# Kernel tuning notes

Measured on AMD Instinct MI355X. Metric: run time of the kernel, lower is better.

The kernel has to match this reference:

```python
import jax, jax.numpy as jnp
import numpy as np
from jax import lax

MU = 0.1          # cfg MODEL.MU (FISTA step size)
LMBD = 0.1        # cfg MODEL.LAMBDA[0]
N_STEPS = 4       # cfg MODEL.NUM_LAYERS (unrolled FISTA iterations)
BN_EPS = 1e-5


def _norm_w(W):
    # DictBlock w_norm: each dictionary filter normalized to unit L2 norm.
    # torch does this under no_grad (in-place on .data), so the norm is a constant.
    n = jnp.sqrt(jnp.sum(W * W, axis=(1, 2, 3), keepdims=True))
    return W / lax.stop_gradient(n + 1e-12)


def _conv(x, W, stride, pad):
    return lax.conv_general_dilated(x, W, (stride, stride), [(pad, pad)] * 2,
                                    dimension_numbers=('NCHW', 'OIHW', 'NCHW'))


def _conv_t(z, W, stride, pad, out_pad):
    # torch conv_transpose2d(z, W, stride, padding=pad, output_padding=out_pad)
    k = W.shape[2]
    Wt = jnp.transpose(jnp.flip(W, (2, 3)), (1, 0, 2, 3))  # (in_ch, dict, k, k)
    p = k - 1 - pad
    return lax.conv_general_dilated(z, Wt, (1, 1), [(p, p + out_pad)] * 2,
                                    lhs_dilation=(stride, stride),
                                    dimension_numbers=('NCHW', 'OIHW', 'NCHW'))


def _shrink(c):
    # non-negative soft threshold: relu(c - lmbd*step)
    return jax.nn.relu(c - LMBD * MU)


def _dict_conv(x, W, stride):
    # Unrolled FISTA sparse coding: min_c 0.5||x - W^T c||^2 + lmbd||c||_1, c>=0
    W = _norm_w(W)
    out_pad = stride - 1
    c = _shrink(MU * _conv(x, W, stride, 1))
    c_pre = jnp.zeros_like(c)
    t = 1.0
    for _ in range(N_STEPS - 1):
        t_next = (1.0 + float(np.sqrt(1.0 + 4.0 * t * t))) / 2.0
        a = c + ((t - 1.0) / t_next) * (c - c_pre)
        c_pre = c
        r = x - _conv_t(a, W, stride, 1, out_pad)       # reconstruction residual
        c = _shrink(a + MU * _conv(r, W, stride, 1))    # proximal gradient step
        t = t_next
    return c


def _bn(x, g, b, m, v):
    # eval-mode BatchNorm2d with running stats
    scale = g * lax.rsqrt(v + BN_EPS)
    return (x - m[None, :, None, None]) * scale[None, :, None, None] + b[None, :, None, None]


def setup_inputs() -> dict:
    key = jax.random.key(0)
    ks = jax.random.split(key, 12)
    N, Cin, Cout, H = 32, 128, 256, 56
    x = jax.random.normal(ks[0], (N, Cin, H, H), jnp.float32)
    def unit_norm(W):
        return W / (jnp.sqrt(jnp.sum(W * W, axis=(1, 2, 3), keepdims=True)) + 1e-12)
    W1 = unit_norm(jax.random.normal(ks[1], (Cout, Cin, 3, 3), jnp.float32))
    W2 = unit_norm(jax.random.normal(ks[2], (Cout, Cout, 3, 3), jnp.float32))
    Wsc = jax.random.normal(ks[3], (Cout, Cin, 1, 1), jnp.float32) * 0.05
    def bn(k):
        k1, k2, k3, k4 = jax.random.split(k, 4)
        g = 1.0 + 0.1 * jax.random.normal(k1, (Cout,), jnp.float32)
        b = 0.1 * jax.random.normal(k2, (Cout,), jnp.float32)
        m = 0.1 * jax.random.normal(k3, (Cout,), jnp.float32)
        v = 0.5 + jax.random.uniform(k4, (Cout,), jnp.float32)
        return g, b, m, v
    bn1_g, bn1_b, bn1_m, bn1_v = bn(ks[4])
    bn2_g, bn2_b, bn2_m, bn2_v = bn(ks[5])
    bnsc_g, bnsc_b, bnsc_m, bnsc_v = bn(ks[6])
    return dict(x=x, W1=W1, W2=W2, Wsc=Wsc,
                bn1_g=bn1_g, bn1_b=bn1_b, bn1_m=bn1_m, bn1_v=bn1_v,
                bn2_g=bn2_g, bn2_b=bn2_b, bn2_m=bn2_m, bn2_v=bn2_v,
                bnsc_g=bnsc_g, bnsc_b=bnsc_b, bnsc_m=bnsc_m, bnsc_v=bnsc_v)


def reference(x, W1, W2, Wsc,
              bn1_g, bn1_b, bn1_m, bn1_v,
              bn2_g, bn2_b, bn2_m, bn2_v,
              bnsc_g, bnsc_b, bnsc_m, bnsc_v):
    out = _bn(_dict_conv(x, W1, 2), bn1_g, bn1_b, bn1_m, bn1_v)
    out = _bn(_dict_conv(out, W2, 1), bn2_g, bn2_b, bn2_m, bn2_v)
    sc = _bn(_conv(x, Wsc, 2, 0), bnsc_g, bnsc_b, bnsc_m, bnsc_v)
    return jax.nn.relu(out + sc)
```

## Files before the change

### kernel.cpp

```cpp
#include <hip/hip_runtime.h>
#include <math.h>

#define MU_F 0.1f
#define SHRINK_F 0.01f
#define BN_EPS_F 1e-5f

typedef _Float16 half_t;
typedef _Float16 half8 __attribute__((ext_vector_type(8)));
typedef float f32x4 __attribute__((ext_vector_type(4)));

#define LROW 40

template<int KS, int S, int PAD, int MODE>
__global__ __launch_bounds__(256, 2)
void conv_big(const half_t* __restrict__ Ag, const half_t* __restrict__ Xh,
              float* __restrict__ outF, half_t* __restrict__ outH,
              const half_t* __restrict__ auxH, const float* __restrict__ auxF,
              int CA, int Cout, int Hin, int Win, int Hout, int Wout, int ptiles,
              float alpha, float beta, float delta, int relu1,
              const float* __restrict__ pscale, const float* __restrict__ pbias,
              const float* __restrict__ aux3, int relu2)
{
    __shared__ __align__(16) half_t sm[2 * 256 * LROW];

    const int tid = threadIdx.x;
    const int wv = tid >> 6, ln = tid & 63;
    const int n = blockIdx.z;
    const int co0 = blockIdx.y * 128;
    const int wco = (wv & 1) * 64, wpx = (wv >> 1) * 64;

    int eh = 0, ew = 0, p0;
    if (MODE == 2) {
        int q = blockIdx.x / ptiles;
        p0 = (blockIdx.x - q * ptiles) * 128;
        eh = q >> 1; ew = q & 1;
    } else {
        p0 = blockIdx.x * 128;
    }

    const int Wd  = (MODE == 2) ? (Wout >> 1) : Wout;
    const int Hd  = (MODE == 2) ? (Hout >> 1) : Hout;
    const int PHW = Hd * Wd;
    const int K9  = KS * KS * CA;

    const int part = tid & 3;
    const int row0 = tid >> 2;

    const size_t abase0 = (size_t)(co0 + row0) * K9 + part * 8;
    const size_t abase1 = abase0 + (size_t)64 * K9;

    int bph[2], bpw[2]; bool bok0[2];
#pragma unroll
    for (int i = 0; i < 2; ++i) {
        int px = p0 + row0 + i * 64;
        bok0[i] = px < PHW;
        int ph = bok0[i] ? (px / Wd) : 0;
        bph[i] = ph; bpw[i] = px - ph * Wd;
    }

    const int cpt = CA >> 5;
    const int lgc = (cpt == 8) ? 3 : 2;
    int ntap, lgj = 0, phh = 0, pww = 0;
    if (MODE == 2) {
        phh = (eh + 1) & 1; pww = (ew + 1) & 1;
        lgj = ew;
        ntap = (1 + eh) * (1 + ew);
    } else {
        ntap = KS * KS;
    }
    const int total = ntap << lgc;

    auto fetch = [&](int flat, half8& a0, half8& a1, half8& b0, half8& b1) {
        const int ci = flat & (cpt - 1);
        const int ti = flat >> lgc;
        int kh, kw;
        if (MODE == 2) {
            int i2 = ti >> lgj, j = ti & ((1 << lgj) - 1);
            kh = phh + 2 * i2; kw = pww + 2 * j;
        } else if (KS == 3) {
            kh = (ti * 11) >> 5; kw = ti - 3 * kh;
        } else { kh = 0; kw = 0; }
        const int c0 = ci << 5;
        const size_t aoff = (size_t)(kh * KS + kw) * CA + c0;
        a0 = *(const half8*)(Ag + abase0 + aoff);
        a1 = *(const half8*)(Ag + abase1 + aoff);
#pragma unroll
        for (int i = 0; i < 2; ++i) {
            bool ok = bok0[i]; int hh, ww2;
            if (MODE == 0) {
                hh = bph[i] * S - PAD + kh; ww2 = bpw[i] * S - PAD + kw;
                ok = ok && (unsigned)hh < (unsigned)Hin && (unsigned)ww2 < (unsigned)Win;
            } else if (MODE == 1) {
                hh = bph[i] + PAD - kh; ww2 = bpw[i] + PAD - kw;
                ok = ok && (unsigned)hh < (unsigned)Hin && (unsigned)ww2 < (unsigned)Win;
            } else {
                int nh = 2 * bph[i] + eh + PAD - kh, nw = 2 * bpw[i] + ew + PAD - kw;
                hh = nh >> 1; ww2 = nw >> 1;
                ok = ok && nh >= 0 && nw >= 0 && hh < Hin && ww2 < Win;
            }
            half8 v = {};
            if (ok) v = *(const half8*)(Xh + ((size_t)(n * Hin + hh) * Win + ww2) * CA + c0 + part * 8);
            if (i == 0) b0 = v; else b1 = v;
        }
    };

    f32x4 acc[4][4] = {};
    half8 pa0, pa1, pb0, pb1;

    fetch(0, pa0, pa1, pb0, pb1);
    {
        half_t* buf = sm;
        *(half8*)(buf +  row0        * LROW + part * 8) = pa0;
        *(half8*)(buf + (row0 +  64) * LROW + part * 8) = pa1;
        *(half8*)(buf + (row0 + 128) * LROW + part * 8) = pb0;
        *(half8*)(buf + (row0 + 192) * LROW + part * 8) = pb1;
    }
    if (total > 1) fetch(1, pa0, pa1, pb0, pb1);
    __syncthreads();

    const int fr = ln & 15, koh = (ln >> 4) * 8;
    for (int k = 0; k < total; ++k) {
        half_t* buf = sm + (k & 1) * (256 * LROW);
        half8 fa[4], fb[4];
#pragma unroll
        for (int m = 0; m < 4; ++m)
            fa[m] = *(const half8*)(buf + (wco + m * 16 + fr) * LROW + koh);
#pragma unroll
        for (int t2 = 0; t2 < 4; ++t2)
            fb[t2] = *(const half8*)(buf + (128 + wpx + t2 * 16 + fr) * LROW + koh);
#pragma unroll
        for (int m = 0; m < 4; ++m)
#pragma unroll
            for (int t2 = 0; t2 < 4; ++t2)
                acc[m][t2] = __builtin_amdgcn_mfma_f32_16x16x32_f16(fa[m], fb[t2], acc[m][t2], 0, 0, 0);
        if (k + 1 < total) {
            half_t* nb = sm + ((k + 1) & 1) * (256 * LROW);
            *(half8*)(nb +  row0        * LROW + part * 8) = pa0;
            *(half8*)(nb + (row0 +  64) * LROW + part * 8) = pa1;
            *(half8*)(nb + (row0 + 128) * LROW + part * 8) = pb0;
            *(half8*)(nb + (row0 + 192) * LROW + part * 8) = pb1;
            if (k + 2 < total) fetch(k + 2, pa0, pa1, pb0, pb1);
            __syncthreads();
        }
    }

    const int rg = ln >> 4;
#pragma unroll
    for (int t = 0; t < 4; ++t) {
        int px = p0 + wpx + t * 16 + fr;
        if (px >= PHW) continue;
        int ph = px / Wd, pw = px - ph * Wd;
        int oh, ow;
        if (MODE == 2) { oh = 2 * ph + eh; ow = 2 * pw + ew; }
        else           { oh = ph;          ow = pw; }
        size_t ghwc = ((size_t)(n * Hout + oh) * Wout + ow) * Cout;
#pragma unroll
        for (int m = 0; m < 4; ++m) {
#pragma unroll
            for (int r = 0; r < 4; ++r) {
                int co_l = co0 + wco + m * 16 + rg * 4 + r;
                size_t fidx = ((size_t)(n * Cout + co_l) * Hout + oh) * Wout + ow;
                float v = alpha * acc[m][t][r] + delta;
                if (auxH) v += beta * (float)auxH[ghwc + co_l];
                if (auxF) v += beta * auxF[fidx];
                if (relu1) v = fmaxf(v, 0.f);
                if (pscale) v = pscale[co_l] * v + pbias[co_l];
                if (aux3) v += aux3[fidx];
                if (relu2) v = fmaxf(v, 0.f);
                if (outH) outH[ghwc + co_l] = (half_t)v;
                else      outF[fidx] = v;
            }
        }
    }
}

template<int KT>
__global__ __launch_bounds__(256)
void pack_w(const float* __restrict__ W, half_t* __restrict__ Wh,
            half_t* __restrict__ WTh, int Cin, int Cout, int do_norm)
{
    __shared__ float red[256];
    int co = blockIdx.x, tid = threadIdx.x;
    int CK = Cin * KT;
    const float* w = W + (size_t)co * CK;
    float inv = 1.f;
    if (do_norm) {
        float s = 0.f;
        for (int i = tid; i < CK; i += 256) { float v = w[i]; s += v * v; }
        red[tid] = s; __syncthreads();
        for (int o = 128; o > 0; o >>= 1) {
            if (tid < o) red[tid] += red[tid + o];
            __syncthreads();
        }
        inv = 1.f / (sqrtf(red[0]) + 1e-12f);
    }
    for (int i = tid; i < CK; i += 256) {
        int ci = i / KT, tap = i - ci * KT;
        half_t h = (half_t)(w[i] * inv);
        Wh[((size_t)co * KT + tap) * Cin + ci] = h;
        if (WTh) WTh[((size_t)ci * KT + tap) * Cout + co] = h;
    }
}

__global__ __launch_bounds__(256)
void tx_kernel(const float* __restrict__ x, half_t* __restrict__ xTh)
{
    __shared__ __align__(16) half_t tl[56 * 136];
    int h = blockIdx.x, n = blockIdx.y, tid = threadIdx.x;
    for (int it = 0; it < 28; ++it) {
        int id = tid + it * 256;
        int c = id / 56, w0 = id - c * 56;
        tl[w0 * 136 + c] = (half_t)x[(((size_t)n * 128 + c) * 56 + h) * 56 + w0];
    }
    __syncthreads();
    if (tid < 224) {
        int w0 = tid >> 2, part = tid & 3;
        size_t base = (((size_t)n * 56 + h) * 56 + w0) * 128 + part * 32;
#pragma unroll
        for (int j = 0; j < 4; ++j)
            *(half8*)(xTh + base + j * 8) = *(const half8*)(tl + w0 * 136 + part * 32 + j * 8);
    }
}

__global__ __launch_bounds__(256)
void comb_kernel(const half_t* __restrict__ c, const half_t* __restrict__ p,
                 half_t* __restrict__ a, float w1, float w2, int n8)
{
    int i = blockIdx.x * 256 + threadIdx.x;
    if (i >= n8) return;
    half8 cv = ((const half8*)c)[i];
    half8 pv = ((const half8*)p)[i];
    half8 r;
#pragma unroll
    for (int j = 0; j < 8; ++j) r[j] = (half_t)(w1 * (float)cv[j] + w2 * (float)pv[j]);
    ((half8*)a)[i] = r;
}

__global__ __launch_bounds__(256)
void bn_prep_kernel(const float* __restrict__ g, const float* __restrict__ b,
                    const float* __restrict__ m, const float* __restrict__ v,
                    float* __restrict__ s, float* __restrict__ t, int C)
{
    int i = blockIdx.x * 256 + threadIdx.x;
    if (i < C) {
        float sc = g[i] * rsqrtf(v[i] + BN_EPS_F);
        s[i] = sc; t[i] = b[i] - m[i] * sc;
    }
}

extern "C" void kernel_launch(void* const* d_in, const int* in_sizes, int n_in,
                              void* d_out, int out_size, void* d_ws, size_t ws_size,
                              hipStream_t stream)
{
    (void)in_sizes; (void)n_in; (void)out_size;
    const float* x    = (const float*)d_in[0];
    const float* W1   = (const float*)d_in[1];
    const float* W2   = (const float*)d_in[2];
    const float* Wsc  = (const float*)d_in[3];
    const float* bn1g = (const float*)d_in[4];
    const float* bn1b = (const float*)d_in[5];
    const float* bn1m = (const float*)d_in[6];
    const float* bn1v = (const float*)d_in[7];
    const float* bn2g = (const float*)d_in[8];
    const float* bn2b = (const float*)d_in[9];
    const float* bn2m = (const float*)d_in[10];
    const float* bn2v = (const float*)d_in[11];
    const float* bscg = (const float*)d_in[12];
    const float* bscb = (const float*)d_in[13];
    const float* bscm = (const float*)d_in[14];
    const float* bscv = (const float*)d_in[15];

    const size_t NB = (size_t)32 * 256 * 28 * 28;
    const size_t NX = (size_t)32 * 128 * 56 * 56;

    char* base = (char*)d_ws;
    size_t off = 0;
    auto alloc = [&](size_t nbytes) -> void* {
        void* r = base + off;
        off = (off + nbytes + 255) & ~(size_t)255;
        return r;
    };
    half_t* Wh1  = (half_t*)alloc(294912 * 2);
    half_t* WTh1 = (half_t*)alloc(294912 * 2);
    half_t* Wh2  = (half_t*)alloc(589824 * 2);
    half_t* WTh2 = (half_t*)alloc(589824 * 2);
    half_t* Wsch = (half_t*)alloc(32768 * 2);
    float* bn1s = (float*)alloc(256 * 4);  float* bn1t = (float*)alloc(256 * 4);
    float* bn2s = (float*)alloc(256 * 4);  float* bn2t = (float*)alloc(256 * 4);
    float* bscs = (float*)alloc(256 * 4);  float* bsct = (float*)alloc(256 * 4);
    half_t* xTh  = (half_t*)alloc(NX * 2);
    half_t* r56h = xTh;
    half_t* Pa   = (half_t*)alloc(NB * 2);
    half_t* Pb   = (half_t*)alloc(NB * 2);
    half_t* Pc   = (half_t*)alloc(NB * 2);
    half_t* Py   = (half_t*)alloc(NB * 2);
    half_t* r28h = (half_t*)alloc(NB * 2);
    float*  scF  = (float*)alloc(NB * 4);
    if (off > ws_size) return;

    float* outp = (float*)d_out;

    double t = 1.0; float al[3];
    for (int i = 0; i < 3; ++i) {
        double tn = (1.0 + sqrt(1.0 + 4.0 * t * t)) / 2.0;
        al[i] = (float)((t - 1.0) / tn); t = tn;
    }

    const dim3 blk(256);
    const dim3 gF(7, 2, 32);
    const dim3 gT2(28, 1, 32);
    const int n8 = (int)(NB / 8);
    const dim3 gC((n8 + 255) / 256);
    const float* NF = nullptr;
    const half_t* NH = nullptr;
    float* NFo = nullptr;
    half_t* NHo = nullptr;

    pack_w<9><<<256, blk, 0, stream>>>(W1, Wh1, WTh1, 128, 256, 1);
    pack_w<9><<<256, blk, 0, stream>>>(W2, Wh2, WTh2, 256, 256, 1);
    pack_w<1><<<256, blk, 0, stream>>>(Wsc, Wsch, nullptr, 128, 256, 0);
    bn_prep_kernel<<<1, blk, 0, stream>>>(bn1g, bn1b, bn1m, bn1v, bn1s, bn1t, 256);
    bn_prep_kernel<<<1, blk, 0, stream>>>(bn2g, bn2b, bn2m, bn2v, bn2s, bn2t, 256);
    bn_prep_kernel<<<1, blk, 0, stream>>>(bscg, bscb, bscm, bscv, bscs, bsct, 256);
    tx_kernel<<<dim3(56, 32), blk, 0, stream>>>(x, xTh);

    conv_big<3,2,1,0><<<gF, blk, 0, stream>>>(Wh1, xTh, NFo, Pa, NH, NF,
        128, 256, 56, 56, 28, 28, 7, MU_F, 0.f, -SHRINK_F, 1, NF, NF, NF, 0);
    conv_big<1,2,0,0><<<gF, blk, 0, stream>>>(Wsch, xTh, scF, NHo, NH, NF,
        128, 256, 56, 56, 28, 28, 7, 1.f, 0.f, 0.f, 0, bscs, bsct, NF, 0);

    conv_big<3,2,1,2><<<gT2, blk, 0, stream>>>(WTh1, Pa, NFo, r56h, NH, x,
        256, 128, 28, 28, 56, 56, 7, -1.f, 1.f, 0.f, 0, NF, NF, NF, 0);
    conv_big<3,2,1,0><<<gF, blk, 0, stream>>>(Wh1, r56h, NFo, Pb, Pa, NF,
        128, 256, 56, 56, 28, 28, 7, MU_F, 1.f, -SHRINK_F, 1, NF, NF, NF, 0);

    comb_kernel<<<gC, blk, 0, stream>>>(Pb, Pa, Pc, 1.f + al[1], -al[1], n8);
    conv_big<3,2,1,2><<<gT2, blk, 0, stream>>>(WTh1, Pc, NFo, r56h, NH, x,
        256, 128, 28, 28, 56, 56, 7, -1.f, 1.f, 0.f, 0, NF, NF, NF, 0);
    conv_big<3,2,1,0><<<gF, blk, 0, stream>>>(Wh1, r56h, NFo, Pa, Pc, NF,
        128, 256, 56, 56, 28, 28, 7, MU_F, 1.f, -SHRINK_F, 1, NF, NF, NF, 0);

    comb_kernel<<<gC, blk, 0, stream>>>(Pa, Pb, Pc, 1.f + al[2], -al[2], n8);
    conv_big<3,2,1,2><<<gT2, blk, 0, stream>>>(WTh1, Pc, NFo, r56h, NH, x,
        256, 128, 28, 28, 56, 56, 7, -1.f, 1.f, 0.f, 0, NF, NF, NF, 0);
    conv_big<3,2,1,0><<<gF, blk, 0, stream>>>(Wh1, r56h, NFo, Py, Pc, NF,
        128, 256, 56, 56, 28, 28, 7, MU_F, 1.f, -SHRINK_F, 1, bn1s, bn1t, NF, 0);

    conv_big<3,1,1,0><<<gF, blk, 0, stream>>>(Wh2, Py, NFo, Pa, NH, NF,
        256, 256, 28, 28, 28, 28, 7, MU_F, 0.f, -SHRINK_F, 1, NF, NF, NF, 0);

    conv_big<3,1,1,1><<<gF, blk, 0, stream>>>(WTh2, Pa, NFo, r28h, Py, NF,
        256, 256, 28, 28, 28, 28, 7, -1.f, 1.f, 0.f, 0, NF, NF, NF, 0);
    conv_big<3,1,1,0><<<gF, blk, 0, stream>>>(Wh2, r28h, NFo, Pb, Pa, NF,
        256, 256, 28, 28, 28, 28, 7, MU_F, 1.f, -SHRINK_F, 1, NF, NF, NF, 0);

    comb_kernel<<<gC, blk, 0, stream>>>(Pb, Pa, Pc, 1.f + al[1], -al[1], n8);
    conv_big<3,1,1,1><<<gF, blk, 0, stream>>>(WTh2, Pc, NFo, r28h, Py, NF,
        256, 256, 28, 28, 28, 28, 7, -1.f, 1.f, 0.f, 0, NF, NF, NF, 0);
    conv_big<3,1,1,0><<<gF, blk, 0, stream>>>(Wh2, r28h, NFo, Pa, Pc, NF,
        256, 256, 28, 28, 28, 28, 7, MU_F, 1.f, -SHRINK_F, 1, NF, NF, NF, 0);

    comb_kernel<<<gC, blk, 0, stream>>>(Pa, Pb, Pc, 1.f + al[2], -al[2], n8);
    conv_big<3,1,1,1><<<gF, blk, 0, stream>>>(WTh2, Pc, NFo, r28h, Py, NF,
        256, 256, 28, 28, 28, 28, 7, -1.f, 1.f, 0.f, 0, NF, NF, NF, 0);
    conv_big<3,1,1,0><<<gF, blk, 0, stream>>>(Wh2, r28h, outp, NHo, Pc, NF,
        256, 256, 28, 28, 28, 28, 7, MU_F, 1.f, -SHRINK_F, 1, bn2s, bn2t, scF, 1);
}
```

Baseline: 1.373 ms.

## Use direct global-to-LDS loads with triple buffering and batch-flattened pixel tiles

Rewrites the implicit-GEMM conv kernel to load A and B tiles straight into LDS with global_load_lds, removing the register staging. It uses a three-stage LDS ring, waits on vmcnt before each barrier, and applies an XOR swizzle to avoid bank conflicts. Pixel tiles now run across the flattened batch: 64 pixels per block, 128 threads, and a remapped block index for locality. Out-of-bounds loads point at a zero page filled by a new kernel. Each block now covers fewer pixels, so there are more blocks and less reuse per block.

```diff
diff --git a/kernel.cpp b/kernel.cpp
--- a/kernel.cpp
+++ b/kernel.cpp
@@ -9,53 +9,76 @@
 typedef _Float16 half8 __attribute__((ext_vector_type(8)));
 typedef float f32x4 __attribute__((ext_vector_type(4)));
 
-#define LROW 40
+__device__ __forceinline__ void gll16(const half_t* g, half_t* l) {
+    __builtin_amdgcn_global_load_lds(
+        (const __attribute__((address_space(1))) void*)g,
+        (__attribute__((address_space(3))) void*)l, 16, 0, 0);
+}
+
+#define VM_WAIT_BARRIER(N) do {                                   \
+    asm volatile("s_waitcnt vmcnt(" #N ")" ::: "memory");         \
+    __builtin_amdgcn_s_barrier();                                 \
+    __builtin_amdgcn_sched_barrier(0);                            \
+} while (0)
 
 template<int KS, int S, int PAD, int MODE>
-__global__ __launch_bounds__(256, 2)
+__global__ __launch_bounds__(128, 2)
 void conv_big(const half_t* __restrict__ Ag, const half_t* __restrict__ Xh,
               float* __restrict__ outF, half_t* __restrict__ outH,
               const half_t* __restrict__ auxH, const float* __restrict__ auxF,
               int CA, int Cout, int Hin, int Win, int Hout, int Wout, int ptiles,
               float alpha, float beta, float delta, int relu1,
               const float* __restrict__ pscale, const float* __restrict__ pbias,
-              const float* __restrict__ aux3, int relu2)
-{
-    __shared__ __align__(16) half_t sm[2 * 256 * LROW];
+              const float* __restrict__ aux3, int relu2,
+              const half_t* __restrict__ zpg)
+{
+    __shared__ __align__(16) half_t sm[3 * 6144];
 
     const int tid = threadIdx.x;
     const int wv = tid >> 6, ln = tid & 63;
-    const int n = blockIdx.z;
     const int co0 = blockIdx.y * 128;
-    const int wco = (wv & 1) * 64, wpx = (wv >> 1) * 64;
+    const int wco = wv * 64;
+
+    int bx = blockIdx.x;
+    {
+        const int cpx = gridDim.x >> 3;
+        bx = (bx & 7) * cpx + (bx >> 3);
+    }
 
     int eh = 0, ew = 0, p0;
     if (MODE == 2) {
-        int q = blockIdx.x / ptiles;
-        p0 = (blockIdx.x - q * ptiles) * 128;
+        int q = bx / ptiles;
+        p0 = (bx - q * ptiles) * 64;
         eh = q >> 1; ew = q & 1;
     } else {
-        p0 = blockIdx.x * 128;
-    }
-
-    const int Wd  = (MODE == 2) ? (Wout >> 1) : Wout;
-    const int Hd  = (MODE == 2) ? (Hout >> 1) : Hout;
-    const int PHW = Hd * Wd;
-    const int K9  = KS * KS * CA;
-
-    const int part = tid & 3;
-    const int row0 = tid >> 2;
-
-    const size_t abase0 = (size_t)(co0 + row0) * K9 + part * 8;
-    const size_t abase1 = abase0 + (size_t)64 * K9;
-
-    int bph[2], bpw[2]; bool bok0[2];
+        p0 = bx * 64;
+    }
+
+    const int Wd   = (MODE == 2) ? (Wout >> 1) : Wout;
+    const int Hd   = (MODE == 2) ? (Hout >> 1) : Hout;
+    const int PHW1 = Hd * Wd;
+    const int NPX  = PHW1 * 32;
+    const int K9   = KS * KS * CA;
+
+    const int r  = tid >> 2;
+    const int s4 = tid & 3;
+    const int sw = (s4 ^ (r & 3)) << 3;
+
+    const size_t abase0 = (size_t)(co0 + r     ) * K9;
+    const size_t abase1 = (size_t)(co0 + r + 32) * K9;
+    const size_t abase2 = (size_t)(co0 + r + 64) * K9;
+    const size_t abase3 = (size_t)(co0 + r + 96) * K9;
+
+    int bph[2], bpw[2]; bool bval[2]; size_t bnb[2];
 #pragma unroll
     for (int i = 0; i < 2; ++i) {
-        int px = p0 + row0 + i * 64;
-        bok0[i] = px < PHW;
-        int ph = bok0[i] ? (px / Wd) : 0;
-        bph[i] = ph; bpw[i] = px - ph * Wd;
+        int px = p0 + i * 32 + r;
+        bval[i] = px < NPX;
+        int pc = bval[i] ? px : 0;
+        int n2 = pc / PHW1; int rem = pc - n2 * PHW1;
+        int ph = rem / Wd;
+        bph[i] = ph; bpw[i] = rem - ph * Wd;
+        bnb[i] = (size_t)n2 * Hin * Win;
     }
 
     const int cpt = CA >> 5;
@@ -70,7 +93,7 @@
     }
     const int total = ntap << lgc;
 
-    auto fetch = [&](int flat, half8& a0, half8& a1, half8& b0, half8& b1) {
+    auto issue = [&](int flat, half_t* dst) {
         const int ci = flat & (cpt - 1);
         const int ti = flat >> lgc;
         int kh, kw;
@@ -81,12 +104,14 @@
             kh = (ti * 11) >> 5; kw = ti - 3 * kh;
         } else { kh = 0; kw = 0; }
         const int c0 = ci << 5;
-        const size_t aoff = (size_t)(kh * KS + kw) * CA + c0;
-        a0 = *(const half8*)(Ag + abase0 + aoff);
-        a1 = *(const half8*)(Ag + abase1 + aoff);
+        const size_t koff = (size_t)(kh * KS + kw) * CA + c0 + sw;
+        gll16(Ag + abase0 + koff, dst +        tid * 8);
+        gll16(Ag + abase1 + koff, dst + 1024 + tid * 8);
+        gll16(Ag + abase2 + koff, dst + 2048 + tid * 8);
+        gll16(Ag + abase3 + koff, dst + 3072 + tid * 8);
 #pragma unroll
         for (int i = 0; i < 2; ++i) {
-            bool ok = bok0[i]; int hh, ww2;
+            int hh, ww2; bool ok = bval[i];
             if (MODE == 0) {
                 hh = bph[i] * S - PAD + kh; ww2 = bpw[i] * S - PAD + kw;
                 ok = ok && (unsigned)hh < (unsigned)Hin && (unsigned)ww2 < (unsigned)Win;
@@ -98,69 +123,68 @@
                 hh = nh >> 1; ww2 = nw >> 1;
                 ok = ok && nh >= 0 && nw >= 0 && hh < Hin && ww2 < Win;
             }
-            half8 v = {};
-            if (ok) v = *(const half8*)(Xh + ((size_t)(n * Hin + hh) * Win + ww2) * CA + c0 + part * 8);
-            if (i == 0) b0 = v; else b1 = v;
+            const half_t* src = ok
+                ? Xh + (bnb[i] + (size_t)(hh * Win + ww2)) * CA + c0 + sw
+                : zpg;
+            gll16(src, dst + 4096 + i * 1024 + tid * 8);
         }
     };
 
     f32x4 acc[4][4] = {};
-    half8 pa0, pa1, pb0, pb1;
-
-    fetch(0, pa0, pa1, pb0, pb1);
-    {
-        half_t* buf = sm;
-        *(half8*)(buf +  row0        * LROW + part * 8) = pa0;
-        *(half8*)(buf + (row0 +  64) * LROW + part * 8) = pa1;
-        *(half8*)(buf + (row0 + 128) * LROW + part * 8) = pb0;
-        *(half8*)(buf + (row0 + 192) * LROW + part * 8) = pb1;
-    }
-    if (total > 1) fetch(1, pa0, pa1, pb0, pb1);
-    __syncthreads();
-
-    const int fr = ln & 15, koh = (ln >> 4) * 8;
+
+    issue(0, sm);
+    issue(1, sm + 6144);
+    VM_WAIT_BARRIER(6);
+
+    const int fr = ln & 15, q8 = ln >> 4;
+    const int rdA = (wco + fr) * 32 + ((q8 ^ (fr & 3)) << 3);
+    const int rdB = (128 + fr) * 32 + ((q8 ^ (fr & 3)) << 3);
+
+    int bi = 0;
     for (int k = 0; k < total; ++k) {
-        half_t* buf = sm + (k & 1) * (256 * LROW);
+        half_t* bufr = sm + bi * 6144;
+        if (k + 2 < total) {
+            int b2 = bi + 2; if (b2 >= 3) b2 -= 3;
+            issue(k + 2, sm + b2 * 6144);
+        }
         half8 fa[4], fb[4];
 #pragma unroll
         for (int m = 0; m < 4; ++m)
-            fa[m] = *(const half8*)(buf + (wco + m * 16 + fr) * LROW + koh);
+            fa[m] = *(const half8*)(bufr + rdA + m * 512);
 #pragma unroll
         for (int t2 = 0; t2 < 4; ++t2)
-            fb[t2] = *(const half8*)(buf + (128 + wpx + t2 * 16 + fr) * LROW + koh);
+            fb[t2] = *(const half8*)(bufr + rdB + t2 * 512);
 #pragma unroll
         for (int m = 0; m < 4; ++m)
 #pragma unroll
             for (int t2 = 0; t2 < 4; ++t2)
                 acc[m][t2] = __builtin_amdgcn_mfma_f32_16x16x32_f16(fa[m], fb[t2], acc[m][t2], 0, 0, 0);
-        if (k + 1 < total) {
-            half_t* nb = sm + ((k + 1) & 1) * (256 * LROW);
-            *(half8*)(nb +  row0        * LROW + part * 8) = pa0;
-            *(half8*)(nb + (row0 +  64) * LROW + part * 8) = pa1;
-            *(half8*)(nb + (row0 + 128) * LROW + part * 8) = pb0;
-            *(half8*)(nb + (row0 + 192) * LROW + part * 8) = pb1;
-            if (k + 2 < total) fetch(k + 2, pa0, pa1, pb0, pb1);
-            __syncthreads();
+        if (k + 2 < total) {
+            VM_WAIT_BARRIER(6);
+        } else if (k + 1 < total) {
+            VM_WAIT_BARRIER(0);
         }
+        bi = (bi == 2) ? 0 : bi + 1;
     }
 
     const int rg = ln >> 4;
 #pragma unroll
     for (int t = 0; t < 4; ++t) {
-        int px = p0 + wpx + t * 16 + fr;
-        if (px >= PHW) continue;
-        int ph = px / Wd, pw = px - ph * Wd;
+        int px = p0 + t * 16 + fr;
+        if (px >= NPX) continue;
+        int n2 = px / PHW1; int rem = px - n2 * PHW1;
+        int ph = rem / Wd, pw = rem - ph * Wd;
         int oh, ow;
         if (MODE == 2) { oh = 2 * ph + eh; ow = 2 * pw + ew; }
         else           { oh = ph;          ow = pw; }
-        size_t ghwc = ((size_t)(n * Hout + oh) * Wout + ow) * Cout;
+        size_t ghwc = ((size_t)(n2 * Hout + oh) * Wout + ow) * Cout;
 #pragma unroll
         for (int m = 0; m < 4; ++m) {
 #pragma unroll
-            for (int r = 0; r < 4; ++r) {
-                int co_l = co0 + wco + m * 16 + rg * 4 + r;
-                size_t fidx = ((size_t)(n * Cout + co_l) * Hout + oh) * Wout + ow;
-                float v = alpha * acc[m][t][r] + delta;
+            for (int rr = 0; rr < 4; ++rr) {
+                int co_l = co0 + wco + m * 16 + rg * 4 + rr;
+                size_t fidx = ((size_t)(n2 * Cout + co_l) * Hout + oh) * Wout + ow;
+                float v = alpha * acc[m][t][rr] + delta;
                 if (auxH) v += beta * (float)auxH[ghwc + co_l];
                 if (auxF) v += beta * auxF[fidx];
                 if (relu1) v = fmaxf(v, 0.f);
@@ -230,10 +254,10 @@
     if (i >= n8) return;
     half8 cv = ((const half8*)c)[i];
     half8 pv = ((const half8*)p)[i];
-    half8 r;
-#pragma unroll
-    for (int j = 0; j < 8; ++j) r[j] = (half_t)(w1 * (float)cv[j] + w2 * (float)pv[j]);
-    ((half8*)a)[i] = r;
+    half8 rres;
+#pragma unroll
+    for (int j = 0; j < 8; ++j) rres[j] = (half_t)(w1 * (float)cv[j] + w2 * (float)pv[j]);
+    ((half8*)a)[i] = rres;
 }
 
 __global__ __launch_bounds__(256)
@@ -246,6 +270,12 @@
         float sc = g[i] * rsqrtf(v[i] + BN_EPS_F);
         s[i] = sc; t[i] = b[i] - m[i] * sc;
     }
+}
+
+__global__ __launch_bounds__(128)
+void zfill_kernel(half_t* __restrict__ p)
+{
+    p[threadIdx.x] = (half_t)0.f;
 }
 
 extern "C" void kernel_launch(void* const* d_in, const int* in_sizes, int n_in,
@@ -288,6 +318,7 @@
     float* bn1s = (float*)alloc(256 * 4);  float* bn1t = (float*)alloc(256 * 4);
     float* bn2s = (float*)alloc(256 * 4);  float* bn2t = (float*)alloc(256 * 4);
     float* bscs = (float*)alloc(256 * 4);  float* bsct = (float*)alloc(256 * 4);
+    half_t* zpg  = (half_t*)alloc(256);
     half_t* xTh  = (half_t*)alloc(NX * 2);
     half_t* r56h = xTh;
     half_t* Pa   = (half_t*)alloc(NB * 2);
@@ -307,8 +338,9 @@
     }
 
     const dim3 blk(256);
-    const dim3 gF(7, 2, 32);
-    const dim3 gT2(28, 1, 32);
+    const dim3 cblk(128);
+    const dim3 gB(392, 2, 1);
+    const dim3 gT2(1568, 1, 1);
     const int n8 = (int)(NB / 8);
     const dim3 gC((n8 + 255) / 256);
     const float* NF = nullptr;
@@ -322,47 +354,48 @@
     bn_prep_kernel<<<1, blk, 0, stream>>>(bn1g, bn1b, bn1m, bn1v, bn1s, bn1t, 256);
     bn_prep_kernel<<<1, blk, 0, stream>>>(bn2g, bn2b, bn2m, bn2v, bn2s, bn2t, 256);
     bn_prep_kernel<<<1, blk, 0, stream>>>(bscg, bscb, bscm, bscv, bscs, bsct, 256);
+    zfill_kernel<<<1, cblk, 0, stream>>>(zpg);
     tx_kernel<<<dim3(56, 32), blk, 0, stream>>>(x, xTh);
 
-    conv_big<3,2,1,0><<<gF, blk, 0, stream>>>(Wh1, xTh, NFo, Pa, NH, NF,
-        128, 256, 56, 56, 28, 28, 7, MU_F, 0.f, -SHRINK_F, 1, NF, NF, NF, 0);
-    conv_big<1,2,0,0><<<gF, blk, 0, stream>>>(Wsch, xTh, scF, NHo, NH, NF,
-        128, 256, 56, 56, 28, 28, 7, 1.f, 0.f, 0.f, 0, bscs, bsct, NF, 0);
-
-    conv_big<3,2,1,2><<<gT2, blk, 0, stream>>>(WTh1, Pa, NFo, r56h, NH, x,
-        256, 128, 28, 28, 56, 56, 7, -1.f, 1.f, 0.f, 0, NF, NF, NF, 0);
-    conv_big<3,2,1,0><<<gF, blk, 0, stream>>>(Wh1, r56h, NFo, Pb, Pa, NF,
-        128, 256, 56, 56, 28, 28, 7, MU_F, 1.f, -SHRINK_F, 1, NF, NF, NF, 0);
+    conv_big<3,2,1,0><<<gB, cblk, 0, stream>>>(Wh1, xTh, NFo, Pa, NH, NF,
+        128, 256, 56, 56, 28, 28, 392, MU_F, 0.f, -SHRINK_F, 1, NF, NF, NF, 0, zpg);
+    conv_big<1,2,0,0><<<gB, cblk, 0, stream>>>(Wsch, xTh, scF, NHo, NH, NF,
+        128, 256, 56, 56, 28, 28, 392, 1.f, 0.f, 0.f, 0, bscs, bsct, NF, 0, zpg);
+
+    conv_big<3,2,1,2><<<gT2, cblk, 0, stream>>>(WTh1, Pa, NFo, r56h, NH, x,
+        256, 128, 28, 28, 56, 56, 392, -1.f, 1.f, 0.f, 0, NF, NF, NF, 0, zpg);
+    conv_big<3,2,1,0><<<gB, cblk, 0, stream>>>(Wh1, r56h, NFo, Pb, Pa, NF,
+        128, 256, 56, 56, 28, 28, 392, MU_F, 1.f, -SHRINK_F, 1, NF, NF, NF, 0, zpg);
 
     comb_kernel<<<gC, blk, 0, stream>>>(Pb, Pa, Pc, 1.f + al[1], -al[1], n8);
-    conv_big<3,2,1,2><<<gT2, blk, 0, stream>>>(WTh1, Pc, NFo, r56h, NH, x,
-        256, 128, 28, 28, 56, 56, 7, -1.f, 1.f, 0.f, 0, NF, NF, NF, 0);
-    conv_big<3,2,1,0><<<gF, blk, 0, stream>>>(Wh1, r56h, NFo, Pa, Pc, NF,
-        128, 256, 56, 56, 28, 28, 7, MU_F, 1.f, -SHRINK_F, 1, NF, NF, NF, 0);
+    conv_big<3,2,1,2><<<gT2, cblk, 0, stream>>>(WTh1, Pc, NFo, r56h, NH, x,
+        256, 128, 28, 28, 56, 56, 392, -1.f, 1.f, 0.f, 0, NF, NF, NF, 0, zpg);
+    conv_big<3,2,1,0><<<gB, cblk, 0, stream>>>(Wh1, r56h, NFo, Pa, Pc, NF,
+        128, 256, 56, 56, 28, 28, 392, MU_F, 1.f, -SHRINK_F, 1, NF, NF, NF, 0, zpg);
 
     comb_kernel<<<gC, blk, 0, stream>>>(Pa, Pb, Pc, 1.f + al[2], -al[2], n8);
-    conv_big<3,2,1,2><<<gT2, blk, 0, stream>>>(WTh1, Pc, NFo, r56h, NH, x,
-        256, 128, 28, 28, 56, 56, 7, -1.f, 1.f, 0.f, 0, NF, NF, NF, 0);
-    conv_big<3,2,1,0><<<gF, blk, 0, stream>>>(Wh1, r56h, NFo, Py, Pc, NF,
-        128, 256, 56, 56, 28, 28, 7, MU_F, 1.f, -SHRINK_F, 1, bn1s, bn1t, NF, 0);
-
-    conv_big<3,1,1,0><<<gF, blk, 0, stream>>>(Wh2, Py, NFo, Pa, NH, NF,
-        256, 256, 28, 28, 28, 28, 7, MU_F, 0.f, -SHRINK_F, 1, NF, NF, NF, 0);
-
-    conv_big<3,1,1,1><<<gF, blk, 0, stream>>>(WTh2, Pa, NFo, r28h, Py, NF,
-        256, 256, 28, 28, 28, 28, 7, -1.f, 1.f, 0.f, 0, NF, NF, NF, 0);
-    conv_big<3,1,1,0><<<gF, blk, 0, stream>>>(Wh2, r28h, NFo, Pb, Pa, NF,
-        256, 256, 28, 28, 28, 28, 7, MU_F, 1.f, -SHRINK_F, 1, NF, NF, NF, 0);
+    conv_big<3,2,1,2><<<gT2, cblk, 0, stream>>>(WTh1, Pc, NFo, r56h, NH, x,
+        256, 128, 28, 28, 56, 56, 392, -1.f, 1.f, 0.f, 0, NF, NF, NF, 0, zpg);
+    conv_big<3,2,1,0><<<gB, cblk, 0, stream>>>(Wh1, r56h, NFo, Py, Pc, NF,
+        128, 256, 56, 56, 28, 28, 392, MU_F, 1.f, -SHRINK_F, 1, bn1s, bn1t, NF, 0, zpg);
+
+    conv_big<3,1,1,0><<<gB, cblk, 0, stream>>>(Wh2, Py, NFo, Pa, NH, NF,
+        256, 256, 28, 28, 28, 28, 392, MU_F, 0.f, -SHRINK_F, 1, NF, NF, NF, 0, zpg);
+
+    conv_big<3,1,1,1><<<gB, cblk, 0, stream>>>(WTh2, Pa, NFo, r28h, Py, NF,
+        256, 256, 28, 28, 28, 28, 392, -1.f, 1.f, 0.f, 0, NF, NF, NF, 0, zpg);
+    conv_big<3,1,1,0><<<gB, cblk, 0, stream>>>(Wh2, r28h, NFo, Pb, Pa, NF,
+        256, 256, 28, 28, 28, 28, 392, MU_F, 1.f, -SHRINK_F, 1, NF, NF, NF, 0, zpg);
 
     comb_kernel<<<gC, blk, 0, stream>>>(Pb, Pa, Pc, 1.f + al[1], -al[1], n8);
-    conv_big<3,1,1,1><<<gF, blk, 0, stream>>>(WTh2, Pc, NFo, r28h, Py, NF,
-        256, 256, 28, 28, 28, 28, 7, -1.f, 1.f, 0.f, 0, NF, NF, NF, 0);
-    conv_big<3,1,1,0><<<gF, blk, 0, stream>>>(Wh2, r28h, NFo, Pa, Pc, NF,
-        256, 256, 28, 28, 28, 28, 7, MU_F, 1.f, -SHRINK_F, 1, NF, NF, NF, 0);
+    conv_big<3,1,1,1><<<gB, cblk, 0, stream>>>(WTh2, Pc, NFo, r28h, Py, NF,
+        256, 256, 28, 28, 28, 28, 392, -1.f, 1.f, 0.f, 0, NF, NF, NF, 0, zpg);
+    conv_big<3,1,1,0><<<gB, cblk, 0, stream>>>(Wh2, r28h, NFo, Pa, Pc, NF,
+        256, 256, 28, 28, 28, 28, 392, MU_F, 1.f, -SHRINK_F, 1, NF, NF, NF, 0, zpg);
 
     comb_kernel<<<gC, blk, 0, stream>>>(Pa, Pb, Pc, 1.f + al[2], -al[2], n8);
-    conv_big<3,1,1,1><<<gF, blk, 0, stream>>>(WTh2, Pc, NFo, r28h, Py, NF,
-        256, 256, 28, 28, 28, 28, 7, -1.f, 1.f, 0.f, 0, NF, NF, NF, 0);
-    conv_big<3,1,1,0><<<gF, blk, 0, stream>>>(Wh2, r28h, outp, NHo, Pc, NF,
-        256, 256, 28, 28, 28, 28, 7, MU_F, 1.f, -SHRINK_F, 1, bn2s, bn2t, scF, 1);
-}
+    conv_big<3,1,1,1><<<gT2.x ? gB : gB, cblk, 0, stream>>>(WTh2, Pc, NFo, r28h, Py, NF,
+        256, 256, 28, 28, 28, 28, 392, -1.f, 1.f, 0.f, 0, NF, NF, NF, 0, zpg);
+    conv_big<3,1,1,0><<<gB, cblk, 0, stream>>>(Wh2, r28h, outp, NHo, Pc, NF,
+        256, 256, 28, 28, 28, 28, 392, MU_F, 1.f, -SHRINK_F, 1, bn2s, bn2t, scF, 1, zpg);
+}
```

Measured after the change: 1.294 ms. 5.8% less time.
